# Kernel optimization log

Hardware: AMD Instinct MI355X
Metric: run time of the kernel (lower is better)

The kernel has to match this reference:

```python
import jax, jax.numpy as jnp
import numpy as np
from jax.experimental.ode import odeint

B, T, H, D = 256, 64, 256, 512
RTOL, ATOL = 1e-3, 1e-4


def setup_inputs() -> dict:
    key = jax.random.key(0)
    ks = jax.random.split(key, 8)
    # shared, strictly increasing timestamps in channel 0
    dt = jax.random.uniform(ks[0], (T,), minval=0.05, maxval=0.15)
    times = jnp.cumsum(dt)
    vals = jax.random.normal(ks[1], (B, T))
    batch = jnp.stack([jnp.broadcast_to(times, (B, T)), vals], axis=-1)  # [B,T,2]
    mask = (jax.random.uniform(ks[2], (B, T)) > 0.2).astype(jnp.float32)
    def lin(k, out_dim, in_dim):
        return jax.random.normal(k, (out_dim, in_dim)) / np.sqrt(in_dim).astype(np.float32)
    return {
        'batch': batch,
        'mask': mask,
        'W1': lin(ks[3], D, H), 'b1': jnp.zeros((D,)),
        'W2': lin(ks[4], H, D), 'b2': jnp.zeros((H,)),
        'W_ih': lin(ks[5], 3 * H, 1), 'b_ih': jnp.zeros((3 * H,)),
        'W_hh': lin(ks[6], 3 * H, H), 'b_hh': jnp.zeros((3 * H,)),
    }


def reference(batch, mask, W1, b1, W2, b2, W_ih, b_ih, W_hh, b_hh):
    def ode_f(h, t):  # tanh(Linear(Linear(h)))
        return jnp.tanh((h @ W1.T + b1) @ W2.T + b2)

    def gru(x, h):  # torch GRUCell math, x: [B,1], h: [B,H]
        gi = x @ W_ih.T + b_ih
        gh = h @ W_hh.T + b_hh
        i_r, i_z, i_n = jnp.split(gi, 3, axis=-1)
        h_r, h_z, h_n = jnp.split(gh, 3, axis=-1)
        r = jax.nn.sigmoid(i_r + h_r)
        z = jax.nn.sigmoid(i_z + h_z)
        n = jnp.tanh(i_n + r * h_n)
        return (1.0 - z) * n + z * h

    times = batch[0, :, 0]                                   # [T]
    t_prev = jnp.concatenate([jnp.zeros((1,), times.dtype), times[:-1]])
    xs = (t_prev, times, batch[:, :, 1].T, mask.T)           # leading axis T
    h0 = jnp.zeros((batch.shape[0], W_hh.shape[1]), batch.dtype)

    def step(h, inp):
        t0, t1, x, m = inp
        hp = odeint(ode_f, h, jnp.stack([t0, t1]), rtol=RTOL, atol=ATOL)[1]
        ht = gru(x[:, None], hp)
        m = m[:, None]
        return m * ht + (1.0 - m) * hp, None

    h, _ = jax.lax.scan(step, h0, xs)
    return h
```

## Files before the change

### kernel.cpp

```cpp
#include <hip/hip_runtime.h>
#include <hip/hip_bf16.h>


#define T_STEPS 64
#define HD 256
#define DD 512
#define NBLK 256

#define WT_B    0u
#define WR_B    131072u
#define WZ_B    262144u
#define WN_B    393216u
#define BTL_B   524288u

typedef _Float16 h2 __attribute__((ext_vector_type(2)));
struct H8 { h2 x, y, z, w; };
union PKU { unsigned int u; _Float16 h[2]; };

__device__ __forceinline__ H8 toH8(uint4 u) { return __builtin_bit_cast(H8, u); }

__device__ __forceinline__ float bf2f(unsigned short h) {
  return __uint_as_float(((unsigned int)h) << 16);
}
__device__ __forceinline__ float ldin(const void* p, int i, bool bf) {
  return bf ? bf2f(((const unsigned short*)p)[i]) : ((const float*)p)[i];
}
__device__ __forceinline__ float fast_tanh(float x) {
  float e = __expf(2.f * x);
  return 1.f - __fdividef(2.f, e + 1.f);
}
__device__ __forceinline__ float fast_sigm(float x) {
  return __fdividef(1.f, 1.f + __expf(-x));
}

#if __has_builtin(__builtin_amdgcn_fdot2)
__device__ __forceinline__ float fdot2(h2 a, h2 b, float c) {
  return __builtin_amdgcn_fdot2(a, b, c, false);
}
#else
__device__ __forceinline__ float fdot2(h2 a, h2 b, float c) {
  return (float)a.x * (float)b.x + ((float)a.y * (float)b.y + c);
}
#endif

__device__ bool detect_bf(const void* batchv) {
  const float* f = (const float*)batchv;
  const unsigned short* u = (const unsigned short*)batchv;
  bool ok32 = true, okbf = true;
  float p32 = 0.f, pbf = 0.f;
#pragma unroll
  for (int t = 0; t < 8; ++t) {
    float v32 = f[2 * t], d32 = v32 - p32;
    if (!(d32 > 0.03f && d32 < 0.17f)) ok32 = false;
    p32 = v32;
    float vbf = bf2f(u[2 * t]), dbf = vbf - pbf;
    if (!(dbf > 0.03f && dbf < 0.17f)) okbf = false;
    pbf = vbf;
  }
  return okbf && !ok32;
}

#define D4H(acc, WH, Y) { \
  acc = fdot2((WH).x, (Y).x, acc); acc = fdot2((WH).y, (Y).y, acc); \
  acc = fdot2((WH).z, (Y).z, acc); acc = fdot2((WH).w, (Y).w, acc); }
#define D4(acc, W, Y) { H8 _wh = toH8(W); D4H(acc, _wh, Y) }

__device__ __forceinline__ uint4 pack8(const float* s) {
  uint4 pk; PKU a, b;
  a.h[0] = (_Float16)s[0]; a.h[1] = (_Float16)s[1]; pk.x = a.u;
  b.h[0] = (_Float16)s[2]; b.h[1] = (_Float16)s[3]; pk.y = b.u;
  a.h[0] = (_Float16)s[4]; a.h[1] = (_Float16)s[5]; pk.z = a.u;
  b.h[0] = (_Float16)s[6]; b.h[1] = (_Float16)s[7]; pk.w = b.u;
  return pk;
}

__global__ void prep_all(const void* __restrict__ batchv,
                         const void* __restrict__ w1v, const void* __restrict__ w2v,
                         const void* __restrict__ b1v, const void* __restrict__ b2v,
                         const void* __restrict__ whhv, float* __restrict__ wsf) {
  __shared__ float w2row[DD];
  __shared__ float2 pacc[4][128];
  __shared__ float wrow[HD];
  __shared__ float bred[8];
  const bool bf = detect_bf(batchv);
  const int o = blockIdx.x;
  const int t = threadIdx.x;

  if (t < 96) {
    const int g = o * 96 + t;
    const int mat = g >> 13;
    const int idx = g & 8191;
    const int rrow = idx >> 5;
    const int m   = idx & 31;
    const int j   = m & 15, kh = m >> 4;
    const int kb  = kh * 128 + j * 8;
    const int srow = mat * 256 + rrow;
    float e[8];
    if (bf) {
      uint4 v = ((const uint4*)whhv)[(srow * HD + kb) >> 3];
      e[0] = bf2f((unsigned short)(v.x & 0xffff)); e[1] = bf2f((unsigned short)(v.x >> 16));
      e[2] = bf2f((unsigned short)(v.y & 0xffff)); e[3] = bf2f((unsigned short)(v.y >> 16));
      e[4] = bf2f((unsigned short)(v.z & 0xffff)); e[5] = bf2f((unsigned short)(v.z >> 16));
      e[6] = bf2f((unsigned short)(v.w & 0xffff)); e[7] = bf2f((unsigned short)(v.w >> 16));
    } else {
      float4 v0 = ((const float4*)whhv)[(srow * HD + kb) >> 2];
      float4 v1 = ((const float4*)whhv)[((srow * HD + kb) >> 2) + 1];
      e[0] = v0.x; e[1] = v0.y; e[2] = v0.z; e[3] = v0.w;
      e[4] = v1.x; e[5] = v1.y; e[6] = v1.z; e[7] = v1.w;
    }
    const unsigned base = (mat == 0) ? WR_B : (mat == 1) ? WZ_B : WN_B;
    const unsigned slot = (unsigned)(j * 512 + ((rrow >> 5) << 6) + ((rrow & 31) << 1) + kh);
    ((uint4*)((char*)wsf + base))[slot] = pack8(e);
  }

  w2row[t] = ldin(w2v, o * DD + t, bf);
  __syncthreads();
  const int kp = t & 127;
  const int h  = t >> 7;
  float a0 = 0.f, a1 = 0.f;
  if (bf) {
    const unsigned int* w1p = (const unsigned int*)w1v;
#pragma unroll 8
    for (int m0 = 0; m0 < 128; ++m0) {
      const int m = h * 128 + m0;
      unsigned int v = w1p[m * 128 + kp];
      const float w = w2row[m];
      a0 += w * bf2f((unsigned short)(v & 0xffff));
      a1 += w * bf2f((unsigned short)(v >> 16));
    }
  } else {
    const float2* w1p = (const float2*)w1v;
#pragma unroll 8
    for (int m0 = 0; m0 < 128; ++m0) {
      const int m = h * 128 + m0;
      float2 v = w1p[m * 128 + kp];
      const float w = w2row[m];
      a0 += w * v.x; a1 += w * v.y;
    }
  }
  pacc[h][kp] = make_float2(a0, a1);
  {
    float p = w2row[t] * ldin(b1v, t, bf);
    p += __shfl_xor(p, 32); p += __shfl_xor(p, 16); p += __shfl_xor(p, 8);
    p += __shfl_xor(p, 4);  p += __shfl_xor(p, 2);  p += __shfl_xor(p, 1);
    if ((t & 63) == 0) bred[t >> 6] = p;
  }
  __syncthreads();
  if (t < 128) {
    float2 s0 = pacc[0][t], s1 = pacc[1][t], s2 = pacc[2][t], s3 = pacc[3][t];
    wrow[2 * t]     = (s0.x + s1.x) + (s2.x + s3.x);
    wrow[2 * t + 1] = (s0.y + s1.y) + (s2.y + s3.y);
  }
  if (t == 0)
    ((float*)((char*)wsf + BTL_B))[o] =
        (bred[0] + bred[1]) + (bred[2] + bred[3]) + (bred[4] + bred[5]) +
        (bred[6] + bred[7]) + ldin(b2v, o, bf);
  __syncthreads();
  if (t < 32) {
    const int j = t & 15, kh = t >> 4;
    const unsigned slot = (unsigned)(j * 512 + ((o >> 5) << 6) + ((o & 31) << 1) + kh);
    ((uint4*)((char*)wsf + WT_B))[slot] = pack8(&wrow[kh * 128 + j * 8]);
  }
}

#define SJ(J, WR, ACC) { H8 yv = toH8(rb[khoff + (J)]); D4(ACC, WR, yv) }
#define STAGE_DOT() ({ float a0 = 0.f, a1 = 0.f, a2 = 0.f, a3 = 0.f; \
  SJ(0,w00,a0) SJ(1,w01,a1) SJ(2,w02,a2) SJ(3,w03,a3) \
  SJ(4,w04,a0) SJ(5,w05,a1) SJ(6,w06,a2) SJ(7,w07,a3) \
  SJ(8,w08,a0) SJ(9,w09,a1) SJ(10,w10,a2) SJ(11,w11,a3) \
  SJ(12,w12,a0) SJ(13,w13,a1) SJ(14,w14,a2) SJ(15,w15,a3) \
  float a = (a0 + a1) + (a2 + a3); a + __shfl_xor(a, 1); })

#define GJ(J, ZR, RR, GZ, GR, GN) { H8 yv = toH8(rb[khoff + (J)]); \
  H8 nv = toH8(nlds[(J) * 512 + tid]); \
  D4(GZ, ZR, yv) D4(GR, RR, yv) D4H(GN, nv, yv) }

#define YIDX(o) (((o) >> 7) * 136 + ((o) & 127))

extern "C" __global__ __launch_bounds__(512)
__attribute__((amdgpu_waves_per_eu(2, 2)))
void ode_rnn_main(const void* __restrict__ batchv, const void* __restrict__ maskv,
                  const void* __restrict__ wihv, const void* __restrict__ bihv,
                  const void* __restrict__ bhhv, const float* __restrict__ wsf,
                  void* __restrict__ outv) {
  extern __shared__ uint4 nlds[];
  __shared__ uint4 ybufA[34], ybufB[34];
  __shared__ float times_s[T_STEPS], xsrow[T_STEPS], msrow[T_STEPS];

  const int tid = threadIdx.x;
  const int w   = tid >> 6;
  const int l   = tid & 63;
  const int o   = w * 32 + (l >> 1);
  const int kh  = l & 1;
  const int khoff = kh * 17;
  const int row = blockIdx.x;
  const bool bf = detect_bf(batchv);

  const uint4* pwt = (const uint4*)((const char*)wsf + WT_B) + tid;
  const uint4* pwz = (const uint4*)((const char*)wsf + WZ_B) + tid;
  uint4 w00 = pwt[0 * 512], w01 = pwt[1 * 512], w02 = pwt[2 * 512], w03 = pwt[3 * 512];
  uint4 w04 = pwt[4 * 512], w05 = pwt[5 * 512], w06 = pwt[6 * 512], w07 = pwt[7 * 512];
  uint4 w08 = pwt[8 * 512], w09 = pwt[9 * 512], w10 = pwt[10 * 512], w11 = pwt[11 * 512];
  uint4 w12 = pwt[12 * 512], w13 = pwt[13 * 512], w14 = pwt[14 * 512], w15 = pwt[15 * 512];
  uint4 z00 = pwz[0 * 512], z01 = pwz[1 * 512], z02 = pwz[2 * 512], z03 = pwz[3 * 512];
  uint4 z04 = pwz[4 * 512], z05 = pwz[5 * 512], z06 = pwz[6 * 512], z07 = pwz[7 * 512];
  uint4 z08 = pwz[8 * 512], z09 = pwz[9 * 512], z10 = pwz[10 * 512], z11 = pwz[11 * 512];
  uint4 z12 = pwz[12 * 512], z13 = pwz[13 * 512], z14 = pwz[14 * 512], z15 = pwz[15 * 512];
  const uint4* pwr = (const uint4*)((const char*)wsf + WR_B) + tid;

  {
    const uint4* src = (const uint4*)((const char*)wsf + WN_B);
#pragma unroll
    for (int i = 0; i < 16; ++i) nlds[i * 512 + tid] = src[i * 512 + tid];
  }

  const float btl_r = ((const float*)((const char*)wsf + BTL_B))[o];
  const float wir = ldin(wihv, o, bf), wiz = ldin(wihv, 256 + o, bf), win = ldin(wihv, 512 + o, bf);
  const float bir = ldin(bihv, o, bf), biz = ldin(bihv, 256 + o, bf), bin_ = ldin(bihv, 512 + o, bf);
  const float bhr = ldin(bhhv, o, bf), bhz = ldin(bhhv, 256 + o, bf), bhn = ldin(bhhv, 512 + o, bf);

  if (tid < T_STEPS) {
    times_s[tid] = ldin(batchv, tid * 2, bf);
    xsrow[tid]   = ldin(batchv, row * (T_STEPS * 2) + tid * 2 + 1, bf);
    msrow[tid]   = ldin(maskv, row * T_STEPS + tid, bf);
  }
  if (tid < 34) { ybufA[tid] = make_uint4(0, 0, 0, 0); ybufB[tid] = make_uint4(0, 0, 0, 0); }
  __syncthreads();

  float yreg = 0.f, kac = 0.f;
  const uint4* rb = ybufA;
  uint4* wbuf = ybufB;

  float tprev = 0.f;
#pragma unroll 1
  for (int step = 0; step < T_STEPS; ++step) {
    const float tcur = times_s[step];
    const float hdt = tcur - tprev;
    tprev = tcur;
    float v, ya;

    v = fast_tanh(STAGE_DOT() + btl_r);
    kac = v;
    ya = yreg + (2.f / 3.f) * hdt * v;
    if (!kh) ((_Float16*)wbuf)[YIDX(o)] = (_Float16)ya;
    __syncthreads();
    { const uint4* t = rb; rb = wbuf; wbuf = (uint4*)t; }

    uint4 rA0 = pwr[0 * 512], rA1 = pwr[1 * 512], rA2 = pwr[2 * 512], rA3 = pwr[3 * 512];
    uint4 rA4 = pwr[4 * 512], rA5 = pwr[5 * 512], rA6 = pwr[6 * 512], rA7 = pwr[7 * 512];

    v = fast_tanh(STAGE_DOT() + btl_r);
    yreg = yreg + hdt * (0.25f * kac + 0.75f * v);
    if (!kh) ((_Float16*)wbuf)[YIDX(o)] = (_Float16)yreg;
    __syncthreads();
    { const uint4* t = rb; rb = wbuf; wbuf = (uint4*)t; }

    {
      uint4 rB0 = pwr[8 * 512], rB1 = pwr[9 * 512], rB2 = pwr[10 * 512], rB3 = pwr[11 * 512];
      uint4 rB4 = pwr[12 * 512], rB5 = pwr[13 * 512], rB6 = pwr[14 * 512], rB7 = pwr[15 * 512];
      float gz0 = 0.f, gz1 = 0.f, gr0 = 0.f, gr1 = 0.f, gn0 = 0.f, gn1 = 0.f;
      GJ(0, z00, rA0, gz0, gr0, gn0) GJ(1, z01, rA1, gz1, gr1, gn1)
      GJ(2, z02, rA2, gz0, gr0, gn0) GJ(3, z03, rA3, gz1, gr1, gn1)
      GJ(4, z04, rA4, gz0, gr0, gn0) GJ(5, z05, rA5, gz1, gr1, gn1)
      GJ(6, z06, rA6, gz0, gr0, gn0) GJ(7, z07, rA7, gz1, gr1, gn1)
      GJ(8, z08, rB0, gz0, gr0, gn0) GJ(9, z09, rB1, gz1, gr1, gn1)
      GJ(10, z10, rB2, gz0, gr0, gn0) GJ(11, z11, rB3, gz1, gr1, gn1)
      GJ(12, z12, rB4, gz0, gr0, gn0) GJ(13, z13, rB5, gz1, gr1, gn1)
      GJ(14, z14, rB6, gz0, gr0, gn0) GJ(15, z15, rB7, gz1, gr1, gn1)
      float gr = gr0 + gr1, gz = gz0 + gz1, gn = gn0 + gn1;
      float Ra = gr + __shfl_xor(gr, 1);
      float Za = gz + __shfl_xor(gz, 1);
      float Na = gn + __shfl_xor(gn, 1);
      const float xv = xsrow[step], mm = msrow[step];
      const float hp = yreg;
      float rr = fast_sigm(xv * wir + bir + Ra + bhr);
      float zz = fast_sigm(xv * wiz + biz + Za + bhz);
      float nn = fast_tanh(xv * win + bin_ + rr * (Na + bhn));
      float ht = (1.f - zz) * nn + zz * hp;
      yreg = mm * ht + (1.f - mm) * hp;
      if (!kh) ((_Float16*)wbuf)[YIDX(o)] = (_Float16)yreg;
      __syncthreads();
      { const uint4* t = rb; rb = wbuf; wbuf = (uint4*)t; }
    }
  }

  if (!kh) {
    int idx = row * HD + o;
    if (bf) ((__hip_bfloat16*)outv)[idx] = __float2bfloat16(yreg);
    else    ((float*)outv)[idx] = yreg;
  }
}

extern "C" void kernel_launch(void* const* d_in, const int* in_sizes, int n_in,
                              void* d_out, int out_size, void* d_ws, size_t ws_size,
                              hipStream_t stream) {
  float* ws = (float*)d_ws;
  prep_all<<<256, 512, 0, stream>>>(d_in[0], d_in[2], d_in[4], d_in[3], d_in[5],
                                    d_in[8], ws);
  (void)hipFuncSetAttribute((const void*)ode_rnn_main,
                            hipFuncAttributeMaxDynamicSharedMemorySize, 131072);
  ode_rnn_main<<<NBLK, 512, 131072, stream>>>(d_in[0], d_in[1], d_in[6], d_in[7], d_in[9],
                                              ws, d_out);
}
```

Baseline: 243.2 us.

## Split each hidden unit's dot products across four lanes with 1024-thread blocks

Doubles the block to 1024 threads so each output unit's 256-wide dot product is split across four lanes instead of two. Each lane now holds half as many weight registers. The weight layouts in the prep kernel and the LDS y-buffer indexing are reorganised to match. The R-gate weight loads move from the ODE stages into the GRU block, and the input and hidden biases are pre-summed. This targets latency in the serial per-step chain, at the cost of an extra shuffle round per reduction and barriers that now span more waves.

```diff
diff --git a/kernel.cpp b/kernel.cpp
--- a/kernel.cpp
+++ b/kernel.cpp
@@ -92,8 +92,7 @@
     const int idx = g & 8191;
     const int rrow = idx >> 5;
     const int m   = idx & 31;
-    const int j   = m & 15, kh = m >> 4;
-    const int kb  = kh * 128 + j * 8;
+    const int kb  = m * 8;
     const int srow = mat * 256 + rrow;
     float e[8];
     if (bf) {
@@ -109,7 +108,8 @@
       e[4] = v1.x; e[5] = v1.y; e[6] = v1.z; e[7] = v1.w;
     }
     const unsigned base = (mat == 0) ? WR_B : (mat == 1) ? WZ_B : WN_B;
-    const unsigned slot = (unsigned)(j * 512 + ((rrow >> 5) << 6) + ((rrow & 31) << 1) + kh);
+    const int j = m & 7, kq = m >> 3;
+    const unsigned slot = (unsigned)(j * 1024 + ((rrow >> 4) << 6) + ((rrow & 15) << 2) + kq);
     ((uint4*)((char*)wsf + base))[slot] = pack8(e);
   }
 
@@ -157,74 +157,72 @@
         (bred[6] + bred[7]) + ldin(b2v, o, bf);
   __syncthreads();
   if (t < 32) {
-    const int j = t & 15, kh = t >> 4;
-    const unsigned slot = (unsigned)(j * 512 + ((o >> 5) << 6) + ((o & 31) << 1) + kh);
-    ((uint4*)((char*)wsf + WT_B))[slot] = pack8(&wrow[kh * 128 + j * 8]);
-  }
-}
-
-#define SJ(J, WR, ACC) { H8 yv = toH8(rb[khoff + (J)]); D4(ACC, WR, yv) }
+    const int j = t & 7, kq = t >> 3;
+    const unsigned slot = (unsigned)(j * 1024 + ((o >> 4) << 6) + ((o & 15) << 2) + kq);
+    ((uint4*)((char*)wsf + WT_B))[slot] = pack8(&wrow[t * 8]);
+  }
+}
+
+#define SJ(J, WR, ACC) { H8 yv = toH8(rb[kqoff + (J)]); D4(ACC, WR, yv) }
 #define STAGE_DOT() ({ float a0 = 0.f, a1 = 0.f, a2 = 0.f, a3 = 0.f; \
   SJ(0,w00,a0) SJ(1,w01,a1) SJ(2,w02,a2) SJ(3,w03,a3) \
   SJ(4,w04,a0) SJ(5,w05,a1) SJ(6,w06,a2) SJ(7,w07,a3) \
-  SJ(8,w08,a0) SJ(9,w09,a1) SJ(10,w10,a2) SJ(11,w11,a3) \
-  SJ(12,w12,a0) SJ(13,w13,a1) SJ(14,w14,a2) SJ(15,w15,a3) \
-  float a = (a0 + a1) + (a2 + a3); a + __shfl_xor(a, 1); })
-
-#define GJ(J, ZR, RR, GZ, GR, GN) { H8 yv = toH8(rb[khoff + (J)]); \
-  H8 nv = toH8(nlds[(J) * 512 + tid]); \
-  D4(GZ, ZR, yv) D4(GR, RR, yv) D4H(GN, nv, yv) }
-
-#define YIDX(o) (((o) >> 7) * 136 + ((o) & 127))
-
-extern "C" __global__ __launch_bounds__(512)
-__attribute__((amdgpu_waves_per_eu(2, 2)))
+  float a = (a0 + a1) + (a2 + a3); \
+  a += __shfl_xor(a, 1); a + __shfl_xor(a, 2); })
+
+#define ZN(J, ZR, GZ, GN) { H8 yv = toH8(rb[kqoff + (J)]); \
+  H8 nv = toH8(nlds[(J) * 1024 + tid]); \
+  D4(GZ, ZR, yv) D4H(GN, nv, yv) }
+#define RJ(J, RR, GR) { H8 yv = toH8(rb[kqoff + (J)]); D4(GR, RR, yv) }
+
+#define YIDX(o) (((o) >> 6) * 72 + ((o) & 63))
+
+extern "C" __global__ __launch_bounds__(1024)
+__attribute__((amdgpu_waves_per_eu(4, 4)))
 void ode_rnn_main(const void* __restrict__ batchv, const void* __restrict__ maskv,
                   const void* __restrict__ wihv, const void* __restrict__ bihv,
                   const void* __restrict__ bhhv, const float* __restrict__ wsf,
                   void* __restrict__ outv) {
   extern __shared__ uint4 nlds[];
-  __shared__ uint4 ybufA[34], ybufB[34];
+  __shared__ uint4 ybufA[36], ybufB[36];
   __shared__ float times_s[T_STEPS], xsrow[T_STEPS], msrow[T_STEPS];
 
   const int tid = threadIdx.x;
+  const int l   = tid & 63;
   const int w   = tid >> 6;
-  const int l   = tid & 63;
-  const int o   = w * 32 + (l >> 1);
-  const int kh  = l & 1;
-  const int khoff = kh * 17;
+  const int o   = w * 16 + (l >> 2);
+  const int kq  = l & 3;
+  const int kqoff = kq * 9;
   const int row = blockIdx.x;
   const bool bf = detect_bf(batchv);
 
   const uint4* pwt = (const uint4*)((const char*)wsf + WT_B) + tid;
   const uint4* pwz = (const uint4*)((const char*)wsf + WZ_B) + tid;
-  uint4 w00 = pwt[0 * 512], w01 = pwt[1 * 512], w02 = pwt[2 * 512], w03 = pwt[3 * 512];
-  uint4 w04 = pwt[4 * 512], w05 = pwt[5 * 512], w06 = pwt[6 * 512], w07 = pwt[7 * 512];
-  uint4 w08 = pwt[8 * 512], w09 = pwt[9 * 512], w10 = pwt[10 * 512], w11 = pwt[11 * 512];
-  uint4 w12 = pwt[12 * 512], w13 = pwt[13 * 512], w14 = pwt[14 * 512], w15 = pwt[15 * 512];
-  uint4 z00 = pwz[0 * 512], z01 = pwz[1 * 512], z02 = pwz[2 * 512], z03 = pwz[3 * 512];
-  uint4 z04 = pwz[4 * 512], z05 = pwz[5 * 512], z06 = pwz[6 * 512], z07 = pwz[7 * 512];
-  uint4 z08 = pwz[8 * 512], z09 = pwz[9 * 512], z10 = pwz[10 * 512], z11 = pwz[11 * 512];
-  uint4 z12 = pwz[12 * 512], z13 = pwz[13 * 512], z14 = pwz[14 * 512], z15 = pwz[15 * 512];
+  uint4 w00 = pwt[0 * 1024], w01 = pwt[1 * 1024], w02 = pwt[2 * 1024], w03 = pwt[3 * 1024];
+  uint4 w04 = pwt[4 * 1024], w05 = pwt[5 * 1024], w06 = pwt[6 * 1024], w07 = pwt[7 * 1024];
+  uint4 z00 = pwz[0 * 1024], z01 = pwz[1 * 1024], z02 = pwz[2 * 1024], z03 = pwz[3 * 1024];
+  uint4 z04 = pwz[4 * 1024], z05 = pwz[5 * 1024], z06 = pwz[6 * 1024], z07 = pwz[7 * 1024];
   const uint4* pwr = (const uint4*)((const char*)wsf + WR_B) + tid;
 
   {
     const uint4* src = (const uint4*)((const char*)wsf + WN_B);
 #pragma unroll
-    for (int i = 0; i < 16; ++i) nlds[i * 512 + tid] = src[i * 512 + tid];
+    for (int i = 0; i < 8; ++i) nlds[i * 1024 + tid] = src[i * 1024 + tid];
   }
 
   const float btl_r = ((const float*)((const char*)wsf + BTL_B))[o];
   const float wir = ldin(wihv, o, bf), wiz = ldin(wihv, 256 + o, bf), win = ldin(wihv, 512 + o, bf);
-  const float bir = ldin(bihv, o, bf), biz = ldin(bihv, 256 + o, bf), bin_ = ldin(bihv, 512 + o, bf);
-  const float bhr = ldin(bhhv, o, bf), bhz = ldin(bhhv, 256 + o, bf), bhn = ldin(bhhv, 512 + o, bf);
+  const float br2 = ldin(bihv, o, bf) + ldin(bhhv, o, bf);
+  const float bz2 = ldin(bihv, 256 + o, bf) + ldin(bhhv, 256 + o, bf);
+  const float bin_ = ldin(bihv, 512 + o, bf);
+  const float bhn  = ldin(bhhv, 512 + o, bf);
 
   if (tid < T_STEPS) {
     times_s[tid] = ldin(batchv, tid * 2, bf);
     xsrow[tid]   = ldin(batchv, row * (T_STEPS * 2) + tid * 2 + 1, bf);
     msrow[tid]   = ldin(maskv, row * T_STEPS + tid, bf);
   }
-  if (tid < 34) { ybufA[tid] = make_uint4(0, 0, 0, 0); ybufB[tid] = make_uint4(0, 0, 0, 0); }
+  if (tid < 36) { ybufA[tid] = make_uint4(0, 0, 0, 0); ybufB[tid] = make_uint4(0, 0, 0, 0); }
   __syncthreads();
 
   float yreg = 0.f, kac = 0.f;
@@ -242,49 +240,45 @@
     v = fast_tanh(STAGE_DOT() + btl_r);
     kac = v;
     ya = yreg + (2.f / 3.f) * hdt * v;
-    if (!kh) ((_Float16*)wbuf)[YIDX(o)] = (_Float16)ya;
+    if (!kq) ((_Float16*)wbuf)[YIDX(o)] = (_Float16)ya;
     __syncthreads();
     { const uint4* t = rb; rb = wbuf; wbuf = (uint4*)t; }
 
-    uint4 rA0 = pwr[0 * 512], rA1 = pwr[1 * 512], rA2 = pwr[2 * 512], rA3 = pwr[3 * 512];
-    uint4 rA4 = pwr[4 * 512], rA5 = pwr[5 * 512], rA6 = pwr[6 * 512], rA7 = pwr[7 * 512];
-
     v = fast_tanh(STAGE_DOT() + btl_r);
     yreg = yreg + hdt * (0.25f * kac + 0.75f * v);
-    if (!kh) ((_Float16*)wbuf)[YIDX(o)] = (_Float16)yreg;
+    if (!kq) ((_Float16*)wbuf)[YIDX(o)] = (_Float16)yreg;
     __syncthreads();
     { const uint4* t = rb; rb = wbuf; wbuf = (uint4*)t; }
 
     {
-      uint4 rB0 = pwr[8 * 512], rB1 = pwr[9 * 512], rB2 = pwr[10 * 512], rB3 = pwr[11 * 512];
-      uint4 rB4 = pwr[12 * 512], rB5 = pwr[13 * 512], rB6 = pwr[14 * 512], rB7 = pwr[15 * 512];
-      float gz0 = 0.f, gz1 = 0.f, gr0 = 0.f, gr1 = 0.f, gn0 = 0.f, gn1 = 0.f;
-      GJ(0, z00, rA0, gz0, gr0, gn0) GJ(1, z01, rA1, gz1, gr1, gn1)
-      GJ(2, z02, rA2, gz0, gr0, gn0) GJ(3, z03, rA3, gz1, gr1, gn1)
-      GJ(4, z04, rA4, gz0, gr0, gn0) GJ(5, z05, rA5, gz1, gr1, gn1)
-      GJ(6, z06, rA6, gz0, gr0, gn0) GJ(7, z07, rA7, gz1, gr1, gn1)
-      GJ(8, z08, rB0, gz0, gr0, gn0) GJ(9, z09, rB1, gz1, gr1, gn1)
-      GJ(10, z10, rB2, gz0, gr0, gn0) GJ(11, z11, rB3, gz1, gr1, gn1)
-      GJ(12, z12, rB4, gz0, gr0, gn0) GJ(13, z13, rB5, gz1, gr1, gn1)
-      GJ(14, z14, rB6, gz0, gr0, gn0) GJ(15, z15, rB7, gz1, gr1, gn1)
+      uint4 rA0 = pwr[0 * 1024], rA1 = pwr[1 * 1024], rA2 = pwr[2 * 1024], rA3 = pwr[3 * 1024];
+      uint4 rB0 = pwr[4 * 1024], rB1 = pwr[5 * 1024], rB2 = pwr[6 * 1024], rB3 = pwr[7 * 1024];
+      float gz0 = 0.f, gz1 = 0.f, gn0 = 0.f, gn1 = 0.f;
+      ZN(0, z00, gz0, gn0) ZN(1, z01, gz1, gn1)
+      ZN(2, z02, gz0, gn0) ZN(3, z03, gz1, gn1)
+      ZN(4, z04, gz0, gn0) ZN(5, z05, gz1, gn1)
+      ZN(6, z06, gz0, gn0) ZN(7, z07, gz1, gn1)
+      float gr0 = 0.f, gr1 = 0.f;
+      RJ(0, rA0, gr0) RJ(1, rA1, gr1) RJ(2, rA2, gr0) RJ(3, rA3, gr1)
+      RJ(4, rB0, gr0) RJ(5, rB1, gr1) RJ(6, rB2, gr0) RJ(7, rB3, gr1)
       float gr = gr0 + gr1, gz = gz0 + gz1, gn = gn0 + gn1;
-      float Ra = gr + __shfl_xor(gr, 1);
-      float Za = gz + __shfl_xor(gz, 1);
-      float Na = gn + __shfl_xor(gn, 1);
+      float Ra = gr + __shfl_xor(gr, 1); Ra += __shfl_xor(Ra, 2);
+      float Za = gz + __shfl_xor(gz, 1); Za += __shfl_xor(Za, 2);
+      float Na = gn + __shfl_xor(gn, 1); Na += __shfl_xor(Na, 2);
       const float xv = xsrow[step], mm = msrow[step];
       const float hp = yreg;
-      float rr = fast_sigm(xv * wir + bir + Ra + bhr);
-      float zz = fast_sigm(xv * wiz + biz + Za + bhz);
+      float rr = fast_sigm(xv * wir + br2 + Ra);
+      float zz = fast_sigm(xv * wiz + bz2 + Za);
       float nn = fast_tanh(xv * win + bin_ + rr * (Na + bhn));
       float ht = (1.f - zz) * nn + zz * hp;
       yreg = mm * ht + (1.f - mm) * hp;
-      if (!kh) ((_Float16*)wbuf)[YIDX(o)] = (_Float16)yreg;
+      if (!kq) ((_Float16*)wbuf)[YIDX(o)] = (_Float16)yreg;
       __syncthreads();
       { const uint4* t = rb; rb = wbuf; wbuf = (uint4*)t; }
     }
   }
 
-  if (!kh) {
+  if (!kq) {
     int idx = row * HD + o;
     if (bf) ((__hip_bfloat16*)outv)[idx] = __float2bfloat16(yreg);
     else    ((float*)outv)[idx] = yreg;
@@ -299,6 +293,6 @@
                                     d_in[8], ws);
   (void)hipFuncSetAttribute((const void*)ode_rnn_main,
                             hipFuncAttributeMaxDynamicSharedMemorySize, 131072);
-  ode_rnn_main<<<NBLK, 512, 131072, stream>>>(d_in[0], d_in[1], d_in[6], d_in[7], d_in[9],
-                                              ws, d_out);
-}
+  ode_rnn_main<<<NBLK, 1024, 131072, stream>>>(d_in[0], d_in[1], d_in[6], d_in[7], d_in[9],
+                                               ws, d_out);
+}
```

New measurement: 365.7 us. 50.4% more time.

## Broadcast hidden state via readlane and split K across wave pairs

Applied to the files above, without the earlier changes.

Reorganises the per-block matvecs so each output row is handled by one lane in two waves, each wave covering half of K. The hidden-state vector is now loaded once per lane from LDS and broadcast with readlane, replacing repeated uint4 LDS reads. Partial sums are combined through shared scratch arrays, which costs an extra barrier per stage. The weight layout in the prep kernel is changed to match. The goal is lower LDS read traffic, but the extra syncs and the readlane scalar traffic may add latency.

```diff
diff --git a/kernel.cpp b/kernel.cpp
--- a/kernel.cpp
+++ b/kernel.cpp
@@ -32,6 +32,9 @@
 __device__ __forceinline__ float fast_sigm(float x) {
   return __fdividef(1.f, 1.f + __expf(-x));
 }
+__device__ __forceinline__ unsigned short f16b(float x) {
+  return __builtin_bit_cast(unsigned short, (_Float16)x);
+}
 
 #if __has_builtin(__builtin_amdgcn_fdot2)
 __device__ __forceinline__ float fdot2(h2 a, h2 b, float c) {
@@ -42,6 +45,10 @@
   return (float)a.x * (float)b.x + ((float)a.y * (float)b.y + c);
 }
 #endif
+
+__device__ __forceinline__ h2 RLH2(unsigned int v, int lane) {
+  return __builtin_bit_cast(h2, __builtin_amdgcn_readlane((int)v, lane));
+}
 
 __device__ bool detect_bf(const void* batchv) {
   const float* f = (const float*)batchv;
@@ -60,11 +67,6 @@
   return okbf && !ok32;
 }
 
-#define D4H(acc, WH, Y) { \
-  acc = fdot2((WH).x, (Y).x, acc); acc = fdot2((WH).y, (Y).y, acc); \
-  acc = fdot2((WH).z, (Y).z, acc); acc = fdot2((WH).w, (Y).w, acc); }
-#define D4(acc, W, Y) { H8 _wh = toH8(W); D4H(acc, _wh, Y) }
-
 __device__ __forceinline__ uint4 pack8(const float* s) {
   uint4 pk; PKU a, b;
   a.h[0] = (_Float16)s[0]; a.h[1] = (_Float16)s[1]; pk.x = a.u;
@@ -92,8 +94,7 @@
     const int idx = g & 8191;
     const int rrow = idx >> 5;
     const int m   = idx & 31;
-    const int j   = m & 15, kh = m >> 4;
-    const int kb  = kh * 128 + j * 8;
+    const int kb  = m * 8;
     const int srow = mat * 256 + rrow;
     float e[8];
     if (bf) {
@@ -109,7 +110,8 @@
       e[4] = v1.x; e[5] = v1.y; e[6] = v1.z; e[7] = v1.w;
     }
     const unsigned base = (mat == 0) ? WR_B : (mat == 1) ? WZ_B : WN_B;
-    const unsigned slot = (unsigned)(j * 512 + ((rrow >> 5) << 6) + ((rrow & 31) << 1) + kh);
+    const unsigned dtid = (unsigned)((((rrow >> 6) * 2 + (m >> 4)) << 6) + (rrow & 63));
+    const unsigned slot = (unsigned)((m & 15) * 512) + dtid;
     ((uint4*)((char*)wsf + base))[slot] = pack8(e);
   }
 
@@ -157,25 +159,29 @@
         (bred[6] + bred[7]) + ldin(b2v, o, bf);
   __syncthreads();
   if (t < 32) {
-    const int j = t & 15, kh = t >> 4;
-    const unsigned slot = (unsigned)(j * 512 + ((o >> 5) << 6) + ((o & 31) << 1) + kh);
-    ((uint4*)((char*)wsf + WT_B))[slot] = pack8(&wrow[kh * 128 + j * 8]);
-  }
-}
-
-#define SJ(J, WR, ACC) { H8 yv = toH8(rb[khoff + (J)]); D4(ACC, WR, yv) }
-#define STAGE_DOT() ({ float a0 = 0.f, a1 = 0.f, a2 = 0.f, a3 = 0.f; \
-  SJ(0,w00,a0) SJ(1,w01,a1) SJ(2,w02,a2) SJ(3,w03,a3) \
-  SJ(4,w04,a0) SJ(5,w05,a1) SJ(6,w06,a2) SJ(7,w07,a3) \
-  SJ(8,w08,a0) SJ(9,w09,a1) SJ(10,w10,a2) SJ(11,w11,a3) \
-  SJ(12,w12,a0) SJ(13,w13,a1) SJ(14,w14,a2) SJ(15,w15,a3) \
-  float a = (a0 + a1) + (a2 + a3); a + __shfl_xor(a, 1); })
-
-#define GJ(J, ZR, RR, GZ, GR, GN) { H8 yv = toH8(rb[khoff + (J)]); \
-  H8 nv = toH8(nlds[(J) * 512 + tid]); \
-  D4(GZ, ZR, yv) D4(GR, RR, yv) D4H(GN, nv, yv) }
-
-#define YIDX(o) (((o) >> 7) * 136 + ((o) & 127))
+    const unsigned dtid = (unsigned)((((o >> 6) * 2 + (t >> 4)) << 6) + (o & 63));
+    const unsigned slot = (unsigned)((t & 15) * 512) + dtid;
+    ((uint4*)((char*)wsf + WT_B))[slot] = pack8(&wrow[t * 8]);
+  }
+}
+
+#define SJ(J, WT) { const int ln = khbase + 2 * (J); \
+  h2 y0 = RLH2(vy.x, ln),     y1 = RLH2(vy.y, ln); \
+  h2 y2 = RLH2(vy.x, ln + 1), y3 = RLH2(vy.y, ln + 1); \
+  H8 wv = toH8(WT); \
+  a0 = fdot2(wv.x, y0, a0); a1 = fdot2(wv.y, y1, a1); \
+  a0 = fdot2(wv.z, y2, a0); a1 = fdot2(wv.w, y3, a1); }
+
+#define GJ(J, ZW, RW) { const int ln = khbase + 2 * (J); \
+  h2 y0 = RLH2(vy.x, ln),     y1 = RLH2(vy.y, ln); \
+  h2 y2 = RLH2(vy.x, ln + 1), y3 = RLH2(vy.y, ln + 1); \
+  H8 zv = toH8(ZW); H8 rv = toH8(RW); H8 nv = toH8(nlds[(J) * 512 + tid]); \
+  gz = fdot2(zv.x, y0, gz); gz = fdot2(zv.y, y1, gz); \
+  gz = fdot2(zv.z, y2, gz); gz = fdot2(zv.w, y3, gz); \
+  gr = fdot2(rv.x, y0, gr); gr = fdot2(rv.y, y1, gr); \
+  gr = fdot2(rv.z, y2, gr); gr = fdot2(rv.w, y3, gr); \
+  gn = fdot2(nv.x, y0, gn); gn = fdot2(nv.y, y1, gn); \
+  gn = fdot2(nv.z, y2, gn); gn = fdot2(nv.w, y3, gn); }
 
 extern "C" __global__ __launch_bounds__(512)
 __attribute__((amdgpu_waves_per_eu(2, 2)))
@@ -184,15 +190,17 @@
                   const void* __restrict__ bhhv, const float* __restrict__ wsf,
                   void* __restrict__ outv) {
   extern __shared__ uint4 nlds[];
-  __shared__ uint4 ybufA[34], ybufB[34];
+  __shared__ __align__(8) unsigned short ybA[256], ybB[256];
+  __shared__ float psf[512];
+  __shared__ float pzf[512], prf[512], pnf[512];
   __shared__ float times_s[T_STEPS], xsrow[T_STEPS], msrow[T_STEPS];
 
   const int tid = threadIdx.x;
+  const int l   = tid & 63;
   const int w   = tid >> 6;
-  const int l   = tid & 63;
-  const int o   = w * 32 + (l >> 1);
-  const int kh  = l & 1;
-  const int khoff = kh * 17;
+  const int khw = w & 1;
+  const int o   = (w >> 1) * 64 + l;
+  const int khbase = __builtin_amdgcn_readfirstlane(khw << 5);
   const int row = blockIdx.x;
   const bool bf = detect_bf(batchv);
 
@@ -216,20 +224,22 @@
 
   const float btl_r = ((const float*)((const char*)wsf + BTL_B))[o];
   const float wir = ldin(wihv, o, bf), wiz = ldin(wihv, 256 + o, bf), win = ldin(wihv, 512 + o, bf);
-  const float bir = ldin(bihv, o, bf), biz = ldin(bihv, 256 + o, bf), bin_ = ldin(bihv, 512 + o, bf);
-  const float bhr = ldin(bhhv, o, bf), bhz = ldin(bhhv, 256 + o, bf), bhn = ldin(bhhv, 512 + o, bf);
+  const float br2 = ldin(bihv, o, bf) + ldin(bhhv, o, bf);
+  const float bz2 = ldin(bihv, 256 + o, bf) + ldin(bhhv, 256 + o, bf);
+  const float bin_ = ldin(bihv, 512 + o, bf);
+  const float bhn  = ldin(bhhv, 512 + o, bf);
 
   if (tid < T_STEPS) {
     times_s[tid] = ldin(batchv, tid * 2, bf);
     xsrow[tid]   = ldin(batchv, row * (T_STEPS * 2) + tid * 2 + 1, bf);
     msrow[tid]   = ldin(maskv, row * T_STEPS + tid, bf);
   }
-  if (tid < 34) { ybufA[tid] = make_uint4(0, 0, 0, 0); ybufB[tid] = make_uint4(0, 0, 0, 0); }
+  if (tid < 256) { ybA[tid] = 0; ybB[tid] = 0; }
   __syncthreads();
 
   float yreg = 0.f, kac = 0.f;
-  const uint4* rb = ybufA;
-  uint4* wbuf = ybufB;
+  const unsigned short* rb = ybA;
+  unsigned short* wbuf = ybB;
 
   float tprev = 0.f;
 #pragma unroll 1
@@ -237,54 +247,78 @@
     const float tcur = times_s[step];
     const float hdt = tcur - tprev;
     tprev = tcur;
-    float v, ya;
-
-    v = fast_tanh(STAGE_DOT() + btl_r);
-    kac = v;
-    ya = yreg + (2.f / 3.f) * hdt * v;
-    if (!kh) ((_Float16*)wbuf)[YIDX(o)] = (_Float16)ya;
-    __syncthreads();
-    { const uint4* t = rb; rb = wbuf; wbuf = (uint4*)t; }
+
+    {
+      const uint2 vy = ((const uint2*)rb)[l];
+      float a0 = 0.f, a1 = 0.f;
+      SJ(0, w00) SJ(1, w01) SJ(2, w02) SJ(3, w03)
+      SJ(4, w04) SJ(5, w05) SJ(6, w06) SJ(7, w07)
+      SJ(8, w08) SJ(9, w09) SJ(10, w10) SJ(11, w11)
+      SJ(12, w12) SJ(13, w13) SJ(14, w14) SJ(15, w15)
+      psf[o + (khw << 8)] = a0 + a1;
+      __syncthreads();
+      if (!khw) {
+        float v = fast_tanh(psf[o] + psf[o + 256] + btl_r);
+        kac = v;
+        wbuf[o] = f16b(yreg + (2.f / 3.f) * hdt * v);
+      }
+      __syncthreads();
+      { const unsigned short* t = rb; rb = wbuf; wbuf = (unsigned short*)t; }
+    }
 
     uint4 rA0 = pwr[0 * 512], rA1 = pwr[1 * 512], rA2 = pwr[2 * 512], rA3 = pwr[3 * 512];
     uint4 rA4 = pwr[4 * 512], rA5 = pwr[5 * 512], rA6 = pwr[6 * 512], rA7 = pwr[7 * 512];
 
-    v = fast_tanh(STAGE_DOT() + btl_r);
-    yreg = yreg + hdt * (0.25f * kac + 0.75f * v);
-    if (!kh) ((_Float16*)wbuf)[YIDX(o)] = (_Float16)yreg;
-    __syncthreads();
-    { const uint4* t = rb; rb = wbuf; wbuf = (uint4*)t; }
-
     {
+      const uint2 vy = ((const uint2*)rb)[l];
+      float a0 = 0.f, a1 = 0.f;
+      SJ(0, w00) SJ(1, w01) SJ(2, w02) SJ(3, w03)
+      SJ(4, w04) SJ(5, w05) SJ(6, w06) SJ(7, w07)
+      SJ(8, w08) SJ(9, w09) SJ(10, w10) SJ(11, w11)
+      SJ(12, w12) SJ(13, w13) SJ(14, w14) SJ(15, w15)
+      psf[o + (khw << 8)] = a0 + a1;
       uint4 rB0 = pwr[8 * 512], rB1 = pwr[9 * 512], rB2 = pwr[10 * 512], rB3 = pwr[11 * 512];
       uint4 rB4 = pwr[12 * 512], rB5 = pwr[13 * 512], rB6 = pwr[14 * 512], rB7 = pwr[15 * 512];
-      float gz0 = 0.f, gz1 = 0.f, gr0 = 0.f, gr1 = 0.f, gn0 = 0.f, gn1 = 0.f;
-      GJ(0, z00, rA0, gz0, gr0, gn0) GJ(1, z01, rA1, gz1, gr1, gn1)
-      GJ(2, z02, rA2, gz0, gr0, gn0) GJ(3, z03, rA3, gz1, gr1, gn1)
-      GJ(4, z04, rA4, gz0, gr0, gn0) GJ(5, z05, rA5, gz1, gr1, gn1)
-      GJ(6, z06, rA6, gz0, gr0, gn0) GJ(7, z07, rA7, gz1, gr1, gn1)
-      GJ(8, z08, rB0, gz0, gr0, gn0) GJ(9, z09, rB1, gz1, gr1, gn1)
-      GJ(10, z10, rB2, gz0, gr0, gn0) GJ(11, z11, rB3, gz1, gr1, gn1)
-      GJ(12, z12, rB4, gz0, gr0, gn0) GJ(13, z13, rB5, gz1, gr1, gn1)
-      GJ(14, z14, rB6, gz0, gr0, gn0) GJ(15, z15, rB7, gz1, gr1, gn1)
-      float gr = gr0 + gr1, gz = gz0 + gz1, gn = gn0 + gn1;
-      float Ra = gr + __shfl_xor(gr, 1);
-      float Za = gz + __shfl_xor(gz, 1);
-      float Na = gn + __shfl_xor(gn, 1);
-      const float xv = xsrow[step], mm = msrow[step];
-      const float hp = yreg;
-      float rr = fast_sigm(xv * wir + bir + Ra + bhr);
-      float zz = fast_sigm(xv * wiz + biz + Za + bhz);
-      float nn = fast_tanh(xv * win + bin_ + rr * (Na + bhn));
-      float ht = (1.f - zz) * nn + zz * hp;
-      yreg = mm * ht + (1.f - mm) * hp;
-      if (!kh) ((_Float16*)wbuf)[YIDX(o)] = (_Float16)yreg;
-      __syncthreads();
-      { const uint4* t = rb; rb = wbuf; wbuf = (uint4*)t; }
-    }
-  }
-
-  if (!kh) {
+      __syncthreads();
+      if (!khw) {
+        float v = fast_tanh(psf[o] + psf[o + 256] + btl_r);
+        yreg = yreg + hdt * (0.25f * kac + 0.75f * v);
+        wbuf[o] = f16b(yreg);
+      }
+      __syncthreads();
+      { const unsigned short* t = rb; rb = wbuf; wbuf = (unsigned short*)t; }
+
+      const uint2 vy2 = ((const uint2*)rb)[l];
+      float gz = 0.f, gr = 0.f, gn = 0.f;
+      { const uint2 vy = vy2;
+        GJ(0, z00, rA0) GJ(1, z01, rA1) GJ(2, z02, rA2) GJ(3, z03, rA3)
+        GJ(4, z04, rA4) GJ(5, z05, rA5) GJ(6, z06, rA6) GJ(7, z07, rA7)
+        GJ(8, z08, rB0) GJ(9, z09, rB1) GJ(10, z10, rB2) GJ(11, z11, rB3)
+        GJ(12, z12, rB4) GJ(13, z13, rB5) GJ(14, z14, rB6) GJ(15, z15, rB7)
+      }
+      pzf[o + (khw << 8)] = gz;
+      prf[o + (khw << 8)] = gr;
+      pnf[o + (khw << 8)] = gn;
+      __syncthreads();
+      if (!khw) {
+        const float Za = pzf[o] + pzf[o + 256];
+        const float Ra = prf[o] + prf[o + 256];
+        const float Na = pnf[o] + pnf[o + 256];
+        const float xv = xsrow[step], mm = msrow[step];
+        const float hp = yreg;
+        float rr = fast_sigm(xv * wir + br2 + Ra);
+        float zz = fast_sigm(xv * wiz + bz2 + Za);
+        float nn = fast_tanh(xv * win + bin_ + rr * (Na + bhn));
+        float ht = (1.f - zz) * nn + zz * hp;
+        yreg = mm * ht + (1.f - mm) * hp;
+        wbuf[o] = f16b(yreg);
+      }
+      __syncthreads();
+      { const unsigned short* t = rb; rb = wbuf; wbuf = (unsigned short*)t; }
+    }
+  }
+
+  if (!khw) {
     int idx = row * HD + o;
     if (bf) ((__hip_bfloat16*)outv)[idx] = __float2bfloat16(yreg);
     else    ((float*)outv)[idx] = yreg;
```

New measurement: 311.3 us. 1.28x slower.
